# Kernel optimization log

Hardware: AMD Instinct MI355X
Metric: run time of the kernel (lower is better)

Reference implementation:

```python
import jax, jax.numpy as jnp
import numpy as np

B, D, DK = 16384, 1024, 1024


def setup_inputs() -> dict:
    key = jax.random.key(0)
    ks = jax.random.split(key, 11)
    return {
        "x": jax.random.normal(ks[0], (B, D), jnp.float32),
        "x_prev": jax.random.normal(ks[1], (B, D), jnp.float32),
        "num": jax.random.uniform(ks[2], (B, DK), jnp.float32),
        "den": jax.random.uniform(ks[3], (B, DK), jnp.float32) + 1.0,
        "Wk": jax.random.normal(ks[4], (DK, D), jnp.float32) * (D ** -0.5),
        "bk": jnp.zeros((DK,), jnp.float32),
        "mix_k": jax.random.uniform(ks[5], (), jnp.float32),
        "Wf": jax.random.normal(ks[6], (D, DK), jnp.float32) * (DK ** -0.5),
        "bf": jnp.zeros((D,), jnp.float32),
        "bonus": jax.random.normal(ks[7], (DK,), jnp.float32) * 0.1,
        "decay": jnp.float32(0.2),
    }


def reference(x, x_prev, num, den, Wk, bk, mix_k, Wf, bf, bonus, decay):
    # MixingLinear: Linear(mix*x + (1-mix)*x_prev). Source uses Kmaker for
    # K, R and V, so all three equal this single projection (faithful to code).
    mixed = mix_k * x + (1.0 - mix_k) * x_prev          # [B, D]
    K = mixed @ Wk.T + bk                                # [B, DK]; K == R == V
    e_bk = jnp.exp(bonus + K)                            # [B, DK]
    wkv = (num + e_bk * K) / (den + e_bk)                # V = K
    rwkv = jax.nn.sigmoid(K) * wkv                       # R = K
    w = jnp.exp(-jnp.exp(decay))                         # scalar time-decay
    eK = jnp.exp(K)
    num_new = w * num + eK * K                           # V = K
    den_new = w * den + eK
    out = rwkv @ Wf.T + bf                               # [B, D]
    return out, num_new, den_new
```

## Files before the change

kernel.cpp:

```cpp
#include <hip/hip_runtime.h>
#include <cstdint>

#define DEV static __device__ __forceinline__

typedef float f32x4 __attribute__((ext_vector_type(4)));
typedef short bf16x8 __attribute__((ext_vector_type(8)));

constexpr int Bsz = 16384;
constexpr int Dd  = 1024;
constexpr int DKd = 1024;

DEV unsigned short f2bf(float f) {
    uint32_t u = __builtin_bit_cast(uint32_t, f);
    u += 0x7FFFu + ((u >> 16) & 1u);
    return (unsigned short)(u >> 16);
}

DEV void async_lds16(const void* g, void* l) {
    __builtin_amdgcn_global_load_lds(
        (const __attribute__((address_space(1))) void*)g,
        (__attribute__((address_space(3))) void*)l,
        16, 0, 0);
}

__global__ void k_prep(const float4* __restrict__ x, const float4* __restrict__ xp,
                       const float* __restrict__ mixp,
                       const float4* __restrict__ Wk, const float4* __restrict__ Wf,
                       unsigned short* __restrict__ mixed,
                       unsigned short* __restrict__ WkB,
                       unsigned short* __restrict__ WfB) {
    constexpr int n_mix = Bsz * Dd / 4;
    constexpr int n_w   = DKd * Dd / 4;
    constexpr int total = n_mix + 2 * n_w;
    const float m = *mixp, m1 = 1.0f - m;
    int i = blockIdx.x * blockDim.x + threadIdx.x;
    const int st = gridDim.x * blockDim.x;
    for (; i < total; i += st) {
        float4 a;
        unsigned short* dst;
        int idx;
        if (i < n_mix) {
            float4 xa = x[i], xb = xp[i];
            a.x = m * xa.x + m1 * xb.x;
            a.y = m * xa.y + m1 * xb.y;
            a.z = m * xa.z + m1 * xb.z;
            a.w = m * xa.w + m1 * xb.w;
            dst = mixed; idx = i;
        } else if (i < n_mix + n_w) {
            a = Wk[i - n_mix]; dst = WkB; idx = i - n_mix;
        } else {
            a = Wf[i - n_mix - n_w]; dst = WfB; idx = i - n_mix - n_w;
        }
        ushort4 o;
        o.x = f2bf(a.x); o.y = f2bf(a.y); o.z = f2bf(a.z); o.w = f2bf(a.w);
        reinterpret_cast<ushort4*>(dst)[idx] = o;
    }
}

template <int EPI>
__global__ __launch_bounds__(256)
void k_gemm(const unsigned short* __restrict__ A,
            const unsigned short* __restrict__ Bw,
            const float* __restrict__ bias,
            const float* __restrict__ num, const float* __restrict__ den,
            const float* __restrict__ bonus, const float* __restrict__ decayp,
            float* __restrict__ o0,
            float* __restrict__ o1,
            unsigned short* __restrict__ orw)
{
    __shared__ __align__(16) unsigned short As[128 * 64];
    __shared__ __align__(16) unsigned short Bs[128 * 64];

    const int tid = threadIdx.x;
    const int bid = (int)blockIdx.x;
    const int cb  = bid & 7;
    const int rb  = bid >> 3;
    const int row0 = rb * 128;
    const int col0 = cb * 128;

    const int lane = tid & 63;
    const int wid  = tid >> 6;
    const int wr = wid >> 1, wc = wid & 1;
    const int l16 = lane & 15, lq = lane >> 4;
    const int xm = l16 & 7;

    const int r0 = tid >> 3;
    const int cg = (tid & 7) ^ (r0 & 7);
    const unsigned short* pa[4];
    const unsigned short* pb[4];
#pragma unroll
    for (int i = 0; i < 4; ++i) {
        pa[i] = A  + (size_t)(row0 + i * 32 + r0) * 1024 + cg * 8;
        pb[i] = Bw + (size_t)(col0 + i * 32 + r0) * 1024 + cg * 8;
    }
    unsigned short* la = &As[tid * 8];
    unsigned short* lb = &Bs[tid * 8];

    const int jj0 = (lq ^ xm) * 8;
    const int jj1 = ((4 + lq) ^ xm) * 8;
    const int aoff0 = (wr * 64 + l16) * 64 + jj0;
    const int aoff1 = (wr * 64 + l16) * 64 + jj1;
    const int boff0 = (wc * 64 + l16) * 64 + jj0;
    const int boff1 = (wc * 64 + l16) * 64 + jj1;

    f32x4 acc[4][4] = {};

#pragma unroll 1
    for (int kt = 0; kt < 16; ++kt) {
        const int ko = kt * 64;
#pragma unroll
        for (int i = 0; i < 4; ++i)
            async_lds16(pa[i] + ko, la + i * 2048);
#pragma unroll
        for (int i = 0; i < 4; ++i)
            async_lds16(pb[i] + ko, lb + i * 2048);
        __syncthreads();

#pragma unroll
        for (int kk = 0; kk < 2; ++kk) {
            const int ao = kk ? aoff1 : aoff0;
            const int bo = kk ? boff1 : boff0;
            bf16x8 af[4], bfr[4];
#pragma unroll
            for (int n = 0; n < 4; ++n)
                bfr[n] = *reinterpret_cast<const bf16x8*>(&Bs[bo + n * 1024]);
#pragma unroll
            for (int m = 0; m < 4; ++m)
                af[m] = *reinterpret_cast<const bf16x8*>(&As[ao + m * 1024]);
#pragma unroll
            for (int m = 0; m < 4; ++m)
#pragma unroll
                for (int n = 0; n < 4; ++n)
                    acc[m][n] = __builtin_amdgcn_mfma_f32_16x16x32_bf16(
                        af[m], bfr[n], acc[m][n], 0, 0, 0);
        }
        __syncthreads();
    }

    const int baserow = row0 + wr * 64 + lq * 4;
    const int basecol = col0 + wc * 64 + l16;

    if constexpr (EPI == 1) {
        const float w_decay = __expf(-__expf(*decayp));
        float cbias[4], cebon[4];
#pragma unroll
        for (int n = 0; n < 4; ++n) {
            cbias[n] = bias[basecol + n * 16];
            cebon[n] = __expf(bonus[basecol + n * 16]);
        }
#pragma unroll
        for (int m = 0; m < 4; ++m) {
#pragma unroll
            for (int r = 0; r < 4; ++r) {
                const size_t rowoff = (size_t)(baserow + m * 16 + r) * 1024;
#pragma unroll
                for (int n = 0; n < 4; ++n) {
                    const size_t idx = rowoff + basecol + n * 16;
                    const float Kv  = acc[m][n][r] + cbias[n];
                    const float eK  = __expf(Kv);
                    const float ebk = cebon[n] * eK;
                    const float nb  = num[idx];
                    const float db  = den[idx];
                    const float wkv = (nb + ebk * Kv) * __builtin_amdgcn_rcpf(db + ebk);
                    const float sig = eK * __builtin_amdgcn_rcpf(1.0f + eK);
                    o0[idx]  = w_decay * nb + eK * Kv;
                    o1[idx]  = w_decay * db + eK;
                    orw[idx] = f2bf(sig * wkv);
                }
            }
        }
    } else {
        float cbias[4];
#pragma unroll
        for (int n = 0; n < 4; ++n) cbias[n] = bias[basecol + n * 16];
#pragma unroll
        for (int m = 0; m < 4; ++m) {
#pragma unroll
            for (int r = 0; r < 4; ++r) {
                const size_t rowoff = (size_t)(baserow + m * 16 + r) * 1024;
#pragma unroll
                for (int n = 0; n < 4; ++n)
                    o0[rowoff + basecol + n * 16] = acc[m][n][r] + cbias[n];
            }
        }
    }
}

extern "C" void kernel_launch(void* const* d_in, const int* in_sizes, int n_in,
                              void* d_out, int out_size, void* d_ws, size_t ws_size,
                              hipStream_t stream) {
    const float* x     = (const float*)d_in[0];
    const float* xprev = (const float*)d_in[1];
    const float* num   = (const float*)d_in[2];
    const float* den   = (const float*)d_in[3];
    const float* Wk    = (const float*)d_in[4];
    const float* bk    = (const float*)d_in[5];
    const float* mixk  = (const float*)d_in[6];
    const float* Wf    = (const float*)d_in[7];
    const float* bf_   = (const float*)d_in[8];
    const float* bonus = (const float*)d_in[9];
    const float* decay = (const float*)d_in[10];

    float* out    = (float*)d_out;
    float* numnew = out + (size_t)Bsz * Dd;
    float* dennew = numnew + (size_t)Bsz * DKd;

    char* ws = (char*)d_ws;
    unsigned short* mixed = (unsigned short*)ws;
    unsigned short* WkB   = (unsigned short*)(ws + (size_t)Bsz * Dd * 2);
    unsigned short* WfB   = WkB + (size_t)DKd * Dd;
    unsigned short* rwkv  = WfB + (size_t)Dd * DKd;

    k_prep<<<2048, 256, 0, stream>>>((const float4*)x, (const float4*)xprev, mixk,
                                     (const float4*)Wk, (const float4*)Wf,
                                     mixed, WkB, WfB);

    const int grid = (Bsz / 128) * (DKd / 128);
    k_gemm<1><<<grid, 256, 0, stream>>>(mixed, WkB, bk, num, den, bonus, decay,
                                        numnew, dennew, rwkv);
    k_gemm<0><<<grid, 256, 0, stream>>>(rwkv, WfB, bf_, nullptr, nullptr, nullptr,
                                        nullptr, out, nullptr, nullptr);
}
```

Baseline: 210.7 us.

## Double-buffer GEMM K-loop with async LDS prefetch and fine-grained vmcnt waits

The GEMM main loop becomes a software pipeline: LDS is split into two buffers, each holding two 32-wide K halves, and global-to-LDS async loads for tile t+2 are issued while tile t is computed. Explicit s_waitcnt vmcnt counts and raw barriers replace the full __syncthreads pair, so compute overlaps memory latency. It also adds launch_bounds occupancy of 2, a new XOR swizzle for the 32-wide rows, and s_setprio around the MFMA block. The risks are correctness of the hand-counted waits and extra register pressure from the occupancy hint.

Result: no change. 211.7 us (+0.5%).

```diff
diff --git a/kernel.cpp b/kernel.cpp
--- a/kernel.cpp
+++ b/kernel.cpp
@@ -2,6 +2,7 @@
 #include <cstdint>
 
 #define DEV static __device__ __forceinline__
+#define WAITVM(N) asm volatile("s_waitcnt vmcnt(" #N ")" ::: "memory")
 
 typedef float f32x4 __attribute__((ext_vector_type(4)));
 typedef short bf16x8 __attribute__((ext_vector_type(8)));
@@ -58,18 +59,17 @@
 }
 
 template <int EPI>
-__global__ __launch_bounds__(256)
+__global__ __launch_bounds__(256, 2)
 void k_gemm(const unsigned short* __restrict__ A,
             const unsigned short* __restrict__ Bw,
             const float* __restrict__ bias,
             const float* __restrict__ num, const float* __restrict__ den,
             const float* __restrict__ bonus, const float* __restrict__ decayp,
-            float* __restrict__ o0,
-            float* __restrict__ o1,
+            float* __restrict__ o0, float* __restrict__ o1,
             unsigned short* __restrict__ orw)
 {
-    __shared__ __align__(16) unsigned short As[128 * 64];
-    __shared__ __align__(16) unsigned short Bs[128 * 64];
+    __shared__ __align__(16) unsigned short As[2][2][128 * 32];
+    __shared__ __align__(16) unsigned short Bs[2][2][128 * 32];
 
     const int tid = threadIdx.x;
     const int bid = (int)blockIdx.x;
@@ -82,60 +82,74 @@
     const int wid  = tid >> 6;
     const int wr = wid >> 1, wc = wid & 1;
     const int l16 = lane & 15, lq = lane >> 4;
-    const int xm = l16 & 7;
-
-    const int r0 = tid >> 3;
-    const int cg = (tid & 7) ^ (r0 & 7);
-    const unsigned short* pa[4];
-    const unsigned short* pb[4];
-#pragma unroll
-    for (int i = 0; i < 4; ++i) {
-        pa[i] = A  + (size_t)(row0 + i * 32 + r0) * 1024 + cg * 8;
-        pb[i] = Bw + (size_t)(col0 + i * 32 + r0) * 1024 + cg * 8;
+
+    const int r1   = tid >> 2;
+    const int glog = (tid & 3) ^ ((tid >> 3) & 3);
+    const unsigned short* pa0 = A  + (size_t)(row0 + r1) * 1024 + glog * 8;
+    const unsigned short* pa1 = A  + (size_t)(row0 + r1 + 64) * 1024 + glog * 8;
+    const unsigned short* pb0 = Bw + (size_t)(col0 + r1) * 1024 + glog * 8;
+    const unsigned short* pb1 = Bw + (size_t)(col0 + r1 + 64) * 1024 + glog * 8;
+
+    const int swz   = (l16 >> 1) & 3;
+    const int abase = (wr * 64 + l16) * 32 + ((lq ^ swz) << 3);
+    const int bbase = (wc * 64 + l16) * 32 + ((lq ^ swz) << 3);
+
+    f32x4 acc[4][4] = {};
+
+    auto stage = [&](int buf, int kk, int t) {
+        const int off = t * 64 + kk * 32;
+        async_lds16(pa0 + off, &As[buf][kk][tid * 8]);
+        async_lds16(pa1 + off, &As[buf][kk][(tid + 256) * 8]);
+        async_lds16(pb0 + off, &Bs[buf][kk][tid * 8]);
+        async_lds16(pb1 + off, &Bs[buf][kk][(tid + 256) * 8]);
+    };
+
+    auto compute = [&](int buf, int kk) {
+        const unsigned short* Ar = &As[buf][kk][abase];
+        const unsigned short* Br = &Bs[buf][kk][bbase];
+        bf16x8 af[4], bfr[4];
+#pragma unroll
+        for (int n = 0; n < 4; ++n)
+            bfr[n] = *reinterpret_cast<const bf16x8*>(Br + n * 512);
+#pragma unroll
+        for (int m = 0; m < 4; ++m)
+            af[m] = *reinterpret_cast<const bf16x8*>(Ar + m * 512);
+        __builtin_amdgcn_s_setprio(1);
+#pragma unroll
+        for (int m = 0; m < 4; ++m)
+#pragma unroll
+            for (int n = 0; n < 4; ++n)
+                acc[m][n] = __builtin_amdgcn_mfma_f32_16x16x32_bf16(
+                    af[m], bfr[n], acc[m][n], 0, 0, 0);
+        __builtin_amdgcn_s_setprio(0);
+    };
+
+    stage(0, 0, 0); stage(0, 1, 0); stage(1, 0, 1); stage(1, 1, 1);
+    WAITVM(12);
+    __builtin_amdgcn_s_barrier();
+    __builtin_amdgcn_sched_barrier(0);
+
+#pragma unroll 1
+    for (int t = 0; t < 14; ++t) {
+        const int buf = t & 1;
+        compute(buf, 0);
+        WAITVM(8);
+        __builtin_amdgcn_s_barrier();
+        __builtin_amdgcn_sched_barrier(0);
+        stage(buf, 0, t + 2);
+        compute(buf, 1);
+        WAITVM(8);
+        __builtin_amdgcn_s_barrier();
+        __builtin_amdgcn_sched_barrier(0);
+        stage(buf, 1, t + 2);
     }
-    unsigned short* la = &As[tid * 8];
-    unsigned short* lb = &Bs[tid * 8];
-
-    const int jj0 = (lq ^ xm) * 8;
-    const int jj1 = ((4 + lq) ^ xm) * 8;
-    const int aoff0 = (wr * 64 + l16) * 64 + jj0;
-    const int aoff1 = (wr * 64 + l16) * 64 + jj1;
-    const int boff0 = (wc * 64 + l16) * 64 + jj0;
-    const int boff1 = (wc * 64 + l16) * 64 + jj1;
-
-    f32x4 acc[4][4] = {};
-
-#pragma unroll 1
-    for (int kt = 0; kt < 16; ++kt) {
-        const int ko = kt * 64;
-#pragma unroll
-        for (int i = 0; i < 4; ++i)
-            async_lds16(pa[i] + ko, la + i * 2048);
-#pragma unroll
-        for (int i = 0; i < 4; ++i)
-            async_lds16(pb[i] + ko, lb + i * 2048);
-        __syncthreads();
-
-#pragma unroll
-        for (int kk = 0; kk < 2; ++kk) {
-            const int ao = kk ? aoff1 : aoff0;
-            const int bo = kk ? boff1 : boff0;
-            bf16x8 af[4], bfr[4];
-#pragma unroll
-            for (int n = 0; n < 4; ++n)
-                bfr[n] = *reinterpret_cast<const bf16x8*>(&Bs[bo + n * 1024]);
-#pragma unroll
-            for (int m = 0; m < 4; ++m)
-                af[m] = *reinterpret_cast<const bf16x8*>(&As[ao + m * 1024]);
-#pragma unroll
-            for (int m = 0; m < 4; ++m)
-#pragma unroll
-                for (int n = 0; n < 4; ++n)
-                    acc[m][n] = __builtin_amdgcn_mfma_f32_16x16x32_bf16(
-                        af[m], bfr[n], acc[m][n], 0, 0, 0);
-        }
-        __syncthreads();
-    }
+    compute(0, 0);
+    WAITVM(8);  __builtin_amdgcn_s_barrier(); __builtin_amdgcn_sched_barrier(0);
+    compute(0, 1);
+    WAITVM(4);  __builtin_amdgcn_s_barrier(); __builtin_amdgcn_sched_barrier(0);
+    compute(1, 0);
+    WAITVM(0);  __builtin_amdgcn_s_barrier(); __builtin_amdgcn_sched_barrier(0);
+    compute(1, 1);
 
     const int baserow = row0 + wr * 64 + lq * 4;
     const int basecol = col0 + wc * 64 + l16;
```
